# Kernel tuning notes

Measured on AMD Instinct MI355X. Metric: run time of the kernel, lower is better.

## Reference

```python
import jax, jax.numpy as jnp
import numpy as np

# tinygemm asymmetric int4 convention
QUANT_MIN, QUANT_MAX = 0, 15
MID_POINT = (QUANT_MAX + QUANT_MIN + 1) / 2.0  # 8.0
OUT_F, IN_F, GROUP = 8192, 8192, 128
M_TOKENS = 64


def setup_inputs() -> dict:
    key = jax.random.key(0)
    kx, kw = jax.random.split(key)
    x = jax.random.normal(kx, (M_TOKENS, IN_F), dtype=jnp.float32)
    # Materialize quantized params exactly as quantize_weight_tinygemm does.
    w = jax.random.normal(kw, (OUT_F, IN_F), dtype=jnp.float32) * 0.02
    ng = IN_F // GROUP
    wg = w.reshape(OUT_F, ng, GROUP)
    min_val = wg.min(axis=2)
    max_val = wg.max(axis=2)
    scale = jnp.maximum((max_val - min_val) / float(QUANT_MAX - QUANT_MIN), 1.1920929e-7)
    zero_point = min_val + scale * MID_POINT
    min_val_recon = zero_point - scale * MID_POINT
    q = jnp.clip(jnp.round((wg - min_val_recon[..., None]) / scale[..., None]),
                 QUANT_MIN, QUANT_MAX).astype(jnp.int32)
    int_data = q.reshape(OUT_F, IN_F)  # values in [0, 15]
    # tinygemm layout: (n_groups, out_features, 2) with [..., 0]=scale, [..., 1]=zero_point
    scale_and_zero = jnp.stack([scale, zero_point], axis=-1).transpose(1, 0, 2)
    return {"x": x, "int_data": int_data, "scale_and_zero": scale_and_zero}


def reference(x, int_data, scale_and_zero):
    # Dequant: w = (q - MID_POINT) * scale + zero_point, per group of GROUP along in_features.
    ng = IN_F // GROUP
    q = int_data.reshape(OUT_F, ng, GROUP).astype(x.dtype)
    scale = scale_and_zero[..., 0].T[:, :, None]       # (OUT_F, ng, 1)
    zero_point = scale_and_zero[..., 1].T[:, :, None]  # (OUT_F, ng, 1)
    w = ((q - MID_POINT) * scale + zero_point).reshape(OUT_F, IN_F)
    return x @ w.T  # (M, OUT_F)
```

## Files before the change

### kernel.cpp

```cpp
#include <hip/hip_runtime.h>


#define OUT_F 8192
#define IN_F  8192
#define M_TOK 64
#define GROUP 128
#define BN    128
#define KSPLIT 16
#define KR    (IN_F / KSPLIT)

typedef short short8 __attribute__((ext_vector_type(8)));
typedef float f32x4  __attribute__((ext_vector_type(4)));
typedef int   int4v  __attribute__((ext_vector_type(4)));

__device__ __forceinline__ int pack_bf2(float lo, float hi) {
    unsigned ul = __float_as_uint(lo) + 0x8000u;
    unsigned uh = __float_as_uint(hi) + 0x8000u;
    return (int)((ul >> 16) | (uh & 0xFFFF0000u));
}

template <bool ATOMIC>
__global__ __launch_bounds__(256, 4)
void woq_gemm(const float* __restrict__ x,
              const int*   __restrict__ qw,
              const float* __restrict__ sz,
              float*       __restrict__ outp) {
    __shared__ int lds_x[16 * 64 * 4];

    const int t    = threadIdx.x;
    const int lane = t & 63;
    const int wv   = t >> 6;
    const int n0   = blockIdx.x * BN;
    const int k0   = blockIdx.y * KR;

    const int nlo  = lane & 15;
    const int quad = lane >> 4;
    const int kq8  = quad << 3;

    const int n1 = n0 + wv * 32 + nlo;
    const int n2 = n1 + 16;

    f32x4 acc[4][2];
#pragma unroll
    for (int mi = 0; mi < 4; ++mi)
#pragma unroll
        for (int ni = 0; ni < 2; ++ni)
            acc[mi][ni] = (f32x4){0.f, 0.f, 0.f, 0.f};

    for (int g = 0; g < KR / GROUP; ++g) {
        const int kg = k0 + g * GROUP;
        const int gg = kg >> 7;

        const float2 p1 = *(const float2*)(sz + ((size_t)gg * OUT_F + n1) * 2);
        const float2 p2 = *(const float2*)(sz + ((size_t)gg * OUT_F + n2) * 2);
        const float s1 = p1.x, c1 = fmaf(-8.f, p1.x, p1.y);
        const float s2 = p2.x, c2 = fmaf(-8.f, p2.x, p2.y);

        __syncthreads();
#pragma unroll
        for (int i = 0; i < 4; ++i) {
            int slot  = t + 256 * i;
            int chunk = slot >> 6;
            int l     = slot & 63;
            int m     = ((chunk & 3) << 4) + (l & 15);
            int kk    = ((chunk >> 2) << 5) + ((l >> 4) << 3);
            const float4* p = (const float4*)(x + (size_t)m * IN_F + kg + kk);
            float4 v0 = p[0];
            float4 v1 = p[1];
            int4v bv;
            bv.x = pack_bf2(v0.x, v0.y);
            bv.y = pack_bf2(v0.z, v0.w);
            bv.z = pack_bf2(v1.x, v1.y);
            bv.w = pack_bf2(v1.z, v1.w);
            *(int4v*)&lds_x[slot * 4] = bv;
        }
        __syncthreads();

#pragma unroll
        for (int ks = 0; ks < 4; ++ks) {
            const int k = kg + ks * 32;

            const int* q1p = qw + (size_t)n1 * IN_F + k + kq8;
            const int* q2p = qw + (size_t)n2 * IN_F + k + kq8;
            const int4 qa = *(const int4*)(q1p);
            const int4 qb = *(const int4*)(q1p + 4);
            const int4 qc = *(const int4*)(q2p);
            const int4 qd = *(const int4*)(q2p + 4);

            short8 a[4];
#pragma unroll
            for (int mi = 0; mi < 4; ++mi)
                a[mi] = *(const short8*)&lds_x[((ks * 4 + mi) * 64 + lane) * 4];

            int4v b1i, b2i;
            b1i.x = pack_bf2(fmaf((float)qa.x, s1, c1), fmaf((float)qa.y, s1, c1));
            b1i.y = pack_bf2(fmaf((float)qa.z, s1, c1), fmaf((float)qa.w, s1, c1));
            b1i.z = pack_bf2(fmaf((float)qb.x, s1, c1), fmaf((float)qb.y, s1, c1));
            b1i.w = pack_bf2(fmaf((float)qb.z, s1, c1), fmaf((float)qb.w, s1, c1));
            short8 b1 = __builtin_bit_cast(short8, b1i);
#pragma unroll
            for (int mi = 0; mi < 4; ++mi)
                acc[mi][0] = __builtin_amdgcn_mfma_f32_16x16x32_bf16(a[mi], b1, acc[mi][0], 0, 0, 0);

            b2i.x = pack_bf2(fmaf((float)qc.x, s2, c2), fmaf((float)qc.y, s2, c2));
            b2i.y = pack_bf2(fmaf((float)qc.z, s2, c2), fmaf((float)qc.w, s2, c2));
            b2i.z = pack_bf2(fmaf((float)qd.x, s2, c2), fmaf((float)qd.y, s2, c2));
            b2i.w = pack_bf2(fmaf((float)qd.z, s2, c2), fmaf((float)qd.w, s2, c2));
            short8 b2 = __builtin_bit_cast(short8, b2i);
#pragma unroll
            for (int mi = 0; mi < 4; ++mi)
                acc[mi][1] = __builtin_amdgcn_mfma_f32_16x16x32_bf16(a[mi], b2, acc[mi][1], 0, 0, 0);
        }
    }

    float* dst = ATOMIC ? outp : outp + (size_t)blockIdx.y * (M_TOK * OUT_F);
#pragma unroll
    for (int mi = 0; mi < 4; ++mi) {
#pragma unroll
        for (int ni = 0; ni < 2; ++ni) {
            const int n = n0 + wv * 32 + ni * 16 + nlo;
#pragma unroll
            for (int r = 0; r < 4; ++r) {
                const int m = mi * 16 + quad * 4 + r;
                if (ATOMIC)
                    atomicAdd(dst + (size_t)m * OUT_F + n, acc[mi][ni][r]);
                else
                    dst[(size_t)m * OUT_F + n] = acc[mi][ni][r];
            }
        }
    }
}

__global__ __launch_bounds__(256)
void woq_reduce(const float* __restrict__ part, float* __restrict__ out) {
    const int i = (blockIdx.x * 256 + threadIdx.x) * 4;
    const size_t stride = (size_t)M_TOK * OUT_F;
    float4 s = *(const float4*)(part + i);
#pragma unroll
    for (int k = 1; k < KSPLIT; ++k) {
        float4 v = *(const float4*)(part + (size_t)k * stride + i);
        s.x += v.x; s.y += v.y; s.z += v.z; s.w += v.w;
    }
    *(float4*)(out + i) = s;
}

extern "C" void kernel_launch(void* const* d_in, const int* in_sizes, int n_in,
                              void* d_out, int out_size, void* d_ws, size_t ws_size,
                              hipStream_t stream) {
    const float* x  = (const float*)d_in[0];
    const int*   qw = (const int*)d_in[1];
    const float* sz = (const float*)d_in[2];
    float* out = (float*)d_out;

    dim3 grid(OUT_F / BN, KSPLIT);
    const size_t need = (size_t)KSPLIT * M_TOK * OUT_F * sizeof(float);

    if (ws_size >= need) {
        float* part = (float*)d_ws;
        woq_gemm<false><<<grid, 256, 0, stream>>>(x, qw, sz, part);
        woq_reduce<<<(M_TOK * OUT_F) / (256 * 4), 256, 0, stream>>>(part, out);
    } else {
        hipMemsetAsync(d_out, 0, (size_t)out_size * sizeof(float), stream);
        woq_gemm<true><<<grid, 256, 0, stream>>>(x, qw, sz, out);
    }
}
```

Baseline: 390.3 us.

## Pre-pack int4 weights into nibbles before the split-K GEMM

Adds a packing kernel that compresses each run of eight int32 quantized weights into one 32-bit word. The GEMM then reads 4-bit packed weights and unpacks them with shifts and masks. This cuts weight traffic in the main GEMM eightfold, but an extra full pass over the int32 weights is added on every call. It also needs more workspace, and falls back to the atomic path if the workspace is too small.

After: 403.8 us. 1.03x slower.

```diff
diff --git a/kernel.cpp b/kernel.cpp
--- a/kernel.cpp
+++ b/kernel.cpp
@@ -8,6 +8,7 @@
 #define BN    128
 #define KSPLIT 16
 #define KR    (IN_F / KSPLIT)
+#define PW_DW (IN_F / 8)
 
 typedef short short8 __attribute__((ext_vector_type(8)));
 typedef float f32x4  __attribute__((ext_vector_type(4)));
@@ -19,12 +20,24 @@
     return (int)((ul >> 16) | (uh & 0xFFFF0000u));
 }
 
-template <bool ATOMIC>
+__global__ __launch_bounds__(256)
+void woq_pack(const int* __restrict__ qw, unsigned* __restrict__ pw) {
+    const int tid = blockIdx.x * 256 + threadIdx.x;
+    const int4* p = (const int4*)(qw + (size_t)tid * 8);
+    int4 a = p[0];
+    int4 b = p[1];
+    unsigned w = (unsigned)a.x        | ((unsigned)a.y << 4)
+               | ((unsigned)a.z << 8) | ((unsigned)a.w << 12)
+               | ((unsigned)b.x << 16)| ((unsigned)b.y << 20)
+               | ((unsigned)b.z << 24)| ((unsigned)b.w << 28);
+    pw[tid] = w;
+}
+
 __global__ __launch_bounds__(256, 4)
-void woq_gemm(const float* __restrict__ x,
-              const int*   __restrict__ qw,
-              const float* __restrict__ sz,
-              float*       __restrict__ outp) {
+void woq_gemm_packed(const float*    __restrict__ x,
+                     const unsigned* __restrict__ pw,
+                     const float*    __restrict__ sz,
+                     float*          __restrict__ outp) {
     __shared__ int lds_x[16 * 64 * 4];
 
     const int t    = threadIdx.x;
@@ -35,10 +48,11 @@
 
     const int nlo  = lane & 15;
     const int quad = lane >> 4;
-    const int kq8  = quad << 3;
 
     const int n1 = n0 + wv * 32 + nlo;
     const int n2 = n1 + 16;
+    const unsigned* pw1 = pw + (size_t)n1 * PW_DW + quad;
+    const unsigned* pw2 = pw + (size_t)n2 * PW_DW + quad;
 
     f32x4 acc[4][2];
 #pragma unroll
@@ -76,59 +90,134 @@
         }
         __syncthreads();
 
+        const int dwg = kg >> 3;
+
+#pragma unroll
+        for (int ks = 0; ks < 4; ++ks) {
+            const unsigned w1 = pw1[dwg + ks * 4];
+            const unsigned w2 = pw2[dwg + ks * 4];
+
+            short8 a[4];
+#pragma unroll
+            for (int mi = 0; mi < 4; ++mi)
+                a[mi] = *(const short8*)&lds_x[((ks * 4 + mi) * 64 + lane) * 4];
+
+            float v1f[8], v2f[8];
+#pragma unroll
+            for (int j = 0; j < 8; ++j) {
+                v1f[j] = fmaf((float)((w1 >> (4 * j)) & 15u), s1, c1);
+                v2f[j] = fmaf((float)((w2 >> (4 * j)) & 15u), s2, c2);
+            }
+            int4v b1i, b2i;
+            b1i.x = pack_bf2(v1f[0], v1f[1]);
+            b1i.y = pack_bf2(v1f[2], v1f[3]);
+            b1i.z = pack_bf2(v1f[4], v1f[5]);
+            b1i.w = pack_bf2(v1f[6], v1f[7]);
+            b2i.x = pack_bf2(v2f[0], v2f[1]);
+            b2i.y = pack_bf2(v2f[2], v2f[3]);
+            b2i.z = pack_bf2(v2f[4], v2f[5]);
+            b2i.w = pack_bf2(v2f[6], v2f[7]);
+            short8 b1 = __builtin_bit_cast(short8, b1i);
+            short8 b2 = __builtin_bit_cast(short8, b2i);
+
+#pragma unroll
+            for (int mi = 0; mi < 4; ++mi) {
+                acc[mi][0] = __builtin_amdgcn_mfma_f32_16x16x32_bf16(a[mi], b1, acc[mi][0], 0, 0, 0);
+                acc[mi][1] = __builtin_amdgcn_mfma_f32_16x16x32_bf16(a[mi], b2, acc[mi][1], 0, 0, 0);
+            }
+        }
+    }
+
+    float* dst = outp + (size_t)blockIdx.y * (M_TOK * OUT_F);
+#pragma unroll
+    for (int mi = 0; mi < 4; ++mi) {
+#pragma unroll
+        for (int ni = 0; ni < 2; ++ni) {
+            const int n = n0 + wv * 32 + ni * 16 + nlo;
+#pragma unroll
+            for (int r = 0; r < 4; ++r) {
+                const int m = mi * 16 + quad * 4 + r;
+                dst[(size_t)m * OUT_F + n] = acc[mi][ni][r];
+            }
+        }
+    }
+}
+
+__global__ __launch_bounds__(256, 4)
+void woq_gemm_atomic(const float* __restrict__ x,
+                     const int*   __restrict__ qw,
+                     const float* __restrict__ sz,
+                     float*       __restrict__ outp) {
+    __shared__ int lds_x[16 * 64 * 4];
+    const int t = threadIdx.x, lane = t & 63, wv = t >> 6;
+    const int n0 = blockIdx.x * BN, k0 = blockIdx.y * KR;
+    const int nlo = lane & 15, quad = lane >> 4, kq8 = quad << 3;
+    const int n1 = n0 + wv * 32 + nlo, n2 = n1 + 16;
+    f32x4 acc[4][2];
+#pragma unroll
+    for (int mi = 0; mi < 4; ++mi)
+#pragma unroll
+        for (int ni = 0; ni < 2; ++ni) acc[mi][ni] = (f32x4){0.f, 0.f, 0.f, 0.f};
+    for (int g = 0; g < KR / GROUP; ++g) {
+        const int kg = k0 + g * GROUP, gg = kg >> 7;
+        const float2 p1 = *(const float2*)(sz + ((size_t)gg * OUT_F + n1) * 2);
+        const float2 p2 = *(const float2*)(sz + ((size_t)gg * OUT_F + n2) * 2);
+        const float s1 = p1.x, c1 = fmaf(-8.f, p1.x, p1.y);
+        const float s2 = p2.x, c2 = fmaf(-8.f, p2.x, p2.y);
+        __syncthreads();
+#pragma unroll
+        for (int i = 0; i < 4; ++i) {
+            int slot = t + 256 * i, chunk = slot >> 6, l = slot & 63;
+            int m = ((chunk & 3) << 4) + (l & 15);
+            int kk = ((chunk >> 2) << 5) + ((l >> 4) << 3);
+            const float4* p = (const float4*)(x + (size_t)m * IN_F + kg + kk);
+            float4 v0 = p[0], v1 = p[1];
+            int4v bv;
+            bv.x = pack_bf2(v0.x, v0.y); bv.y = pack_bf2(v0.z, v0.w);
+            bv.z = pack_bf2(v1.x, v1.y); bv.w = pack_bf2(v1.z, v1.w);
+            *(int4v*)&lds_x[slot * 4] = bv;
+        }
+        __syncthreads();
 #pragma unroll
         for (int ks = 0; ks < 4; ++ks) {
             const int k = kg + ks * 32;
-
             const int* q1p = qw + (size_t)n1 * IN_F + k + kq8;
             const int* q2p = qw + (size_t)n2 * IN_F + k + kq8;
-            const int4 qa = *(const int4*)(q1p);
-            const int4 qb = *(const int4*)(q1p + 4);
-            const int4 qc = *(const int4*)(q2p);
-            const int4 qd = *(const int4*)(q2p + 4);
-
+            const int4 qa = *(const int4*)(q1p), qb = *(const int4*)(q1p + 4);
+            const int4 qc = *(const int4*)(q2p), qd = *(const int4*)(q2p + 4);
             short8 a[4];
 #pragma unroll
             for (int mi = 0; mi < 4; ++mi)
                 a[mi] = *(const short8*)&lds_x[((ks * 4 + mi) * 64 + lane) * 4];
-
             int4v b1i, b2i;
             b1i.x = pack_bf2(fmaf((float)qa.x, s1, c1), fmaf((float)qa.y, s1, c1));
             b1i.y = pack_bf2(fmaf((float)qa.z, s1, c1), fmaf((float)qa.w, s1, c1));
             b1i.z = pack_bf2(fmaf((float)qb.x, s1, c1), fmaf((float)qb.y, s1, c1));
             b1i.w = pack_bf2(fmaf((float)qb.z, s1, c1), fmaf((float)qb.w, s1, c1));
-            short8 b1 = __builtin_bit_cast(short8, b1i);
-#pragma unroll
-            for (int mi = 0; mi < 4; ++mi)
-                acc[mi][0] = __builtin_amdgcn_mfma_f32_16x16x32_bf16(a[mi], b1, acc[mi][0], 0, 0, 0);
-
             b2i.x = pack_bf2(fmaf((float)qc.x, s2, c2), fmaf((float)qc.y, s2, c2));
             b2i.y = pack_bf2(fmaf((float)qc.z, s2, c2), fmaf((float)qc.w, s2, c2));
             b2i.z = pack_bf2(fmaf((float)qd.x, s2, c2), fmaf((float)qd.y, s2, c2));
             b2i.w = pack_bf2(fmaf((float)qd.z, s2, c2), fmaf((float)qd.w, s2, c2));
+            short8 b1 = __builtin_bit_cast(short8, b1i);
             short8 b2 = __builtin_bit_cast(short8, b2i);
 #pragma unroll
-            for (int mi = 0; mi < 4; ++mi)
+            for (int mi = 0; mi < 4; ++mi) {
+                acc[mi][0] = __builtin_amdgcn_mfma_f32_16x16x32_bf16(a[mi], b1, acc[mi][0], 0, 0, 0);
                 acc[mi][1] = __builtin_amdgcn_mfma_f32_16x16x32_bf16(a[mi], b2, acc[mi][1], 0, 0, 0);
-        }
-    }
-
-    float* dst = ATOMIC ? outp : outp + (size_t)blockIdx.y * (M_TOK * OUT_F);
-#pragma unroll
-    for (int mi = 0; mi < 4; ++mi) {
+            }
+        }
+    }
+#pragma unroll
+    for (int mi = 0; mi < 4; ++mi)
 #pragma unroll
         for (int ni = 0; ni < 2; ++ni) {
             const int n = n0 + wv * 32 + ni * 16 + nlo;
 #pragma unroll
             for (int r = 0; r < 4; ++r) {
                 const int m = mi * 16 + quad * 4 + r;
-                if (ATOMIC)
-                    atomicAdd(dst + (size_t)m * OUT_F + n, acc[mi][ni][r]);
-                else
-                    dst[(size_t)m * OUT_F + n] = acc[mi][ni][r];
-            }
-        }
-    }
+                atomicAdd(outp + (size_t)m * OUT_F + n, acc[mi][ni][r]);
+            }
+        }
 }
 
 __global__ __launch_bounds__(256)
@@ -152,15 +241,18 @@
     const float* sz = (const float*)d_in[2];
     float* out = (float*)d_out;
 
+    const size_t pw_bytes   = (size_t)OUT_F * PW_DW * sizeof(unsigned);
+    const size_t part_bytes = (size_t)KSPLIT * M_TOK * OUT_F * sizeof(float);
     dim3 grid(OUT_F / BN, KSPLIT);
-    const size_t need = (size_t)KSPLIT * M_TOK * OUT_F * sizeof(float);
-
-    if (ws_size >= need) {
-        float* part = (float*)d_ws;
-        woq_gemm<false><<<grid, 256, 0, stream>>>(x, qw, sz, part);
+
+    if (ws_size >= pw_bytes + part_bytes) {
+        unsigned* pw  = (unsigned*)d_ws;
+        float*    part = (float*)((char*)d_ws + pw_bytes);
+        woq_pack<<<(OUT_F * PW_DW) / 256, 256, 0, stream>>>(qw, pw);
+        woq_gemm_packed<<<grid, 256, 0, stream>>>(x, pw, sz, part);
         woq_reduce<<<(M_TOK * OUT_F) / (256 * 4), 256, 0, stream>>>(part, out);
     } else {
         hipMemsetAsync(d_out, 0, (size_t)out_size * sizeof(float), stream);
-        woq_gemm<true><<<grid, 256, 0, stream>>>(x, qw, sz, out);
-    }
-}
+        woq_gemm_atomic<<<grid, 256, 0, stream>>>(x, qw, sz, out);
+    }
+}
```
